# Optimization experiments

Measured on AMD Instinct MI355X. Metric: run time of the kernel, lower is better.

Reference implementation:

```python
import jax, jax.numpy as jnp
import numpy as np

STRIDES = (4, 8, 16, 32, 64, 128)
MAPS = (128, 64, 32, 16, 8, 4)
VAR0, VAR1 = 0.1, 0.2
CLS_TH, NMS_TH, FINAL_TH = 0.05, 0.3, 0.5


def _decode_scale(ocls, oreg, stride):
    # ocls: [1,2,H,W], oreg: [1,4,H,W] -> dets [H*W, 5] = (x1,y1,x2,y2,score)
    prob = jax.nn.softmax(ocls, axis=1)[0, 1]          # [H,W] face probability
    H, W = prob.shape
    s = jnp.float32(stride)
    pcx = s / 2 + jnp.arange(W, dtype=jnp.float32)[None, :] * s   # prior center x
    pcy = s / 2 + jnp.arange(H, dtype=jnp.float32)[:, None] * s   # prior center y
    pwh = s * 4.0                                                 # prior w = h = 4*stride
    loc = oreg[0]                                                 # [4,H,W]
    cx = pcx + loc[0] * VAR0 * pwh
    cy = pcy + loc[1] * VAR0 * pwh
    w = pwh * jnp.exp(loc[2] * VAR1)
    h = pwh * jnp.exp(loc[3] * VAR1)
    x1 = cx - w / 2
    y1 = cy - h / 2
    x2 = x1 + w
    y2 = y1 + h
    return jnp.stack([x1.ravel(), y1.ravel(), x2.ravel(), y2.ravel(), prob.ravel()], axis=1)


def _nms_keep(dets, valid):
    # Greedy NMS (torch-style, +1 box convention), fixed trip count, returns keep mask.
    N = dets.shape[0]
    scores = jnp.where(valid, dets[:, 4], -jnp.inf)
    order = jnp.argsort(-scores)            # descending by score, invalid last
    b = dets[order]
    v = valid[order]
    x1, y1, x2, y2 = b[:, 0], b[:, 1], b[:, 2], b[:, 3]
    areas = (x2 - x1 + 1.0) * (y2 - y1 + 1.0)
    pos = jnp.arange(N)

    def body(i, carry):
        sup, keep = carry
        active = jnp.logical_and(jnp.logical_not(sup[i]), v[i])
        keep = keep.at[i].set(active)
        xx1 = jnp.maximum(x1[i], x1)
        yy1 = jnp.maximum(y1[i], y1)
        xx2 = jnp.minimum(x2[i], x2)
        yy2 = jnp.minimum(y2[i], y2)
        w = jnp.maximum(xx2 - xx1 + 1.0, 0.0)
        h = jnp.maximum(yy2 - yy1 + 1.0, 0.0)
        inter = w * h
        iou = inter / (areas[i] + areas - inter)
        sup = sup | (active & (iou > NMS_TH) & (pos > i))
        return sup, keep

    sup0 = jnp.logical_not(v)
    _, keep_sorted = jax.lax.fori_loop(0, N, body, (sup0, jnp.zeros(N, dtype=bool)))
    return jnp.zeros(N, dtype=bool).at[order].set(keep_sorted)


def _forward(ol1, ol2, ol3, ol4, ol5, ol6, ol7, ol8, ol9, ol10, ol11, ol12):
    olist = [ol1, ol2, ol3, ol4, ol5, ol6, ol7, ol8, ol9, ol10, ol11, ol12]
    dets = jnp.concatenate(
        [_decode_scale(olist[2 * i], olist[2 * i + 1], STRIDES[i]) for i in range(6)],
        axis=0)                              # [N,5]
    valid = dets[:, 4] > CLS_TH              # threshold stage (score > 0.05)
    # NMS selection is index logic -> constant w.r.t. differentiation
    keep = _nms_keep(jax.lax.stop_gradient(dets), valid)
    final = keep & (dets[:, 4] > FINAL_TH)   # post-NMS score > 0.5 filter
    # fixed-shape equivalent of gathering kept rows: zero out non-kept rows
    return dets * final[:, None].astype(dets.dtype)


def setup_inputs() -> dict:
    key = jax.random.key(0)
    inp = {}
    for i, hw in enumerate(MAPS):
        kc, kr, key = jax.random.split(key, 3)
        inp[f"ol{2 * i + 1}"] = jax.random.normal(kc, (1, 2, hw, hw), dtype=jnp.float32)
        inp[f"ol{2 * i + 2}"] = jax.random.normal(kr, (1, 4, hw, hw), dtype=jnp.float32)
    return inp


def reference(ol1, ol2, ol3, ol4, ol5, ol6, ol7, ol8, ol9, ol10, ol11, ol12):
    return _forward(ol1, ol2, ol3, ol4, ol5, ol6, ol7, ol8, ol9, ol10, ol11, ol12)
```

## Files before the change

kernel.cpp:

```cpp
#include <hip/hip_runtime.h>
#include <stdint.h>

#define N_TOTAL 21840
#define NA      21888
#define W_MAX   342
#define TOT_ENT 3753792u
#define NMS_TH  0.3f
#define FINAL_TH 0.5f
#define NSLICE  8
#define SLOTS   11
#define SCAN_T  768
#define GRP     4
#define NBAND   7

struct Inputs { const float* cls[6]; const float* reg[6]; };

__device__ __forceinline__ void block_bar() {
  asm volatile("s_waitcnt lgkmcnt(0)\n\ts_barrier" ::: "memory");
}

__device__ __forceinline__ unsigned rowbase_u(unsigned r) {
  unsigned w = r >> 6, l = r & 63u;
  return 64u * (342u * w - (w * (w - 1u)) / 2u) + l * (342u - w);
}

__global__ void decode_kernel(Inputs in,
                              float* __restrict__ dx1, float* __restrict__ dy1,
                              float* __restrict__ dx2, float* __restrict__ dy2,
                              float* __restrict__ dsc,
                              unsigned long long* __restrict__ ckey,
                              unsigned int* __restrict__ Mc,
                              unsigned int* __restrict__ rank32,
                              unsigned int* __restrict__ cnt,
                              float* __restrict__ out) {
#pragma clang fp contract(off)
  int gid = blockIdx.x * blockDim.x + threadIdx.x;
  if (gid >= N_TOTAL) return;

  rank32[gid] = 0u;
  cnt[gid] = 0u;
  if (gid < NA - N_TOTAL) cnt[N_TOTAL + gid] = 0u;

  int sc, local;
  if      (gid < 16384) { sc = 0; local = gid;         }
  else if (gid < 20480) { sc = 1; local = gid - 16384; }
  else if (gid < 21504) { sc = 2; local = gid - 20480; }
  else if (gid < 21760) { sc = 3; local = gid - 21504; }
  else if (gid < 21824) { sc = 4; local = gid - 21760; }
  else                  { sc = 5; local = gid - 21824; }

  const int Wd     = 128 >> sc;
  const int stride = 4 << sc;
  const int HW     = Wd * Wd;
  const int x = local & (Wd - 1);
  const int y = local >> (7 - sc);

  const float* cls = in.cls[sc];
  const float* reg = in.reg[sc];

  float c0 = cls[local];
  float c1 = cls[HW + local];
  float m  = fmaxf(c0, c1);
  float e0 = expf(c0 - m);
  float e1 = expf(c1 - m);
  float prob = e1 / (e0 + e1);

  float l0 = reg[local];
  float l1 = reg[HW + local];
  float l2 = reg[2 * HW + local];
  float l3 = reg[3 * HW + local];

  float sF  = (float)stride;
  float pcx = 0.5f * sF + (float)x * sF;
  float pcy = 0.5f * sF + (float)y * sF;
  float pwh = sF * 4.0f;

  float cx = pcx + ((l0 * 0.1f) * pwh);
  float cy = pcy + ((l1 * 0.1f) * pwh);
  float w  = pwh * expf(l2 * 0.2f);
  float h  = pwh * expf(l3 * 0.2f);
  float x1 = cx - w * 0.5f;
  float y1 = cy - h * 0.5f;
  float x2 = x1 + w;
  float y2 = y1 + h;

  dx1[gid] = x1; dy1[gid] = y1; dx2[gid] = x2; dy2[gid] = y2; dsc[gid] = prob;

  out[gid * 5 + 0] = 0.0f;
  out[gid * 5 + 1] = 0.0f;
  out[gid * 5 + 2] = 0.0f;
  out[gid * 5 + 3] = 0.0f;
  out[gid * 5 + 4] = 0.0f;

  if (prob > FINAL_TH) {
    unsigned int pos = atomicAdd(Mc, 1u);
    ckey[pos] = ((unsigned long long)__float_as_uint(prob) << 32) |
                (unsigned int)(~(unsigned int)gid);
  }
}

__global__ void __launch_bounds__(256)
rank_kernel(const unsigned long long* __restrict__ ckey,
            const unsigned int* __restrict__ Mc,
            const float* __restrict__ dx1, const float* __restrict__ dy1,
            const float* __restrict__ dx2, const float* __restrict__ dy2,
            float* __restrict__ sx1, float* __restrict__ sy1,
            float* __restrict__ sx2, float* __restrict__ sy2,
            unsigned int* __restrict__ sorig,
            unsigned int* __restrict__ rank32) {
  __shared__ unsigned long long tile[256];
  const unsigned int M = *Mc;
  if (blockIdx.x * 256u >= M) return;
  const int t = (int)threadIdx.x;
  const int p = (int)blockIdx.x * 256 + t;
  unsigned long long mykey = (p < (int)M) ? ckey[p] : 0ull;
  const int S  = (int)((M + NSLICE - 1) / NSLICE);
  const int lo = (int)blockIdx.y * S;
  const int hi = min((int)M, lo + S);
  int partial = 0;
  const int nt = (hi > lo) ? ((hi - lo + 255) >> 8) : 0;
  for (int ti = 0; ti < nt; ++ti) {
    int j = lo + ti * 256 + t;
    tile[t] = (j < hi) ? ckey[j] : 0ull;
    __syncthreads();
#pragma unroll 8
    for (int q = 0; q < 256; ++q) partial += (tile[q] > mykey) ? 1 : 0;
    __syncthreads();
  }
  if (p < (int)M) {
    unsigned int pack = (unsigned int)partial | (1u << 24);
    unsigned int old  = atomicAdd(&rank32[p], pack);
    unsigned int newv = old + pack;
    if ((newv >> 24) == NSLICE) {
      int r = (int)(newv & 0xFFFFFF);
      unsigned int orig = ~(unsigned int)(mykey & 0xffffffffull);
      sx1[r] = dx1[orig];
      sy1[r] = dy1[orig];
      sx2[r] = dx2[orig];
      sy2[r] = dy2[orig];
      sorig[r] = orig;
    }
  }
}

__global__ void __launch_bounds__(1024)
pairs_kernel(const float* __restrict__ sx1, const float* __restrict__ sy1,
             const float* __restrict__ sx2, const float* __restrict__ sy2,
             const unsigned int* __restrict__ Mc,
             unsigned long long* __restrict__ diag,
             unsigned long long* __restrict__ bandT,
             unsigned int* __restrict__ cnt,
             unsigned short* __restrict__ rlJw,
             unsigned long long* __restrict__ rlBits) {
#pragma clang fp contract(off)
  const int M = (int)*Mc;
  const int W = (M + 63) >> 6;
  const int rw = (int)blockIdx.y;
  const int cwg = (int)blockIdx.x << 4;
  if (rw >= W || cwg >= W || cwg + 22 < rw) return;

  const int t = (int)threadIdx.x;
  const int g = t >> 6, l = t & 63;
  const int cw = cwg + g;

  __shared__ float cx1[1024], cy1[1024], cx2[1024], cy2[1024], car[1024];
  {
    int c = (cw << 6) + l;
    if (cw < W && c < M) {
      float a = sx1[c], b = sy1[c], d = sx2[c], e = sy2[c];
      cx1[t] = a; cy1[t] = b; cx2[t] = d; cy2[t] = e;
      car[t] = (d - a + 1.0f) * (e - b + 1.0f);
    }
  }
  __syncthreads();
  if (cw >= W) return;
  const int rwg = rw >> 2, cg = cw >> 2;
  const bool isDiag = (cw == rw);
  const bool isBand = (cw < rw) && (cg >= rwg - 1);
  const bool isCsr  = (cg >= rwg + 2);
  if (!isDiag && !isBand && !isCsr) return;

  const int r = (rw << 6) + l;
  unsigned long long bits = 0ull;
  if (r < M) {
    float ax1 = sx1[r], ay1 = sy1[r], ax2 = sx2[r], ay2 = sy2[r];
    float aarea = (ax2 - ax1 + 1.0f) * (ay2 - ay1 + 1.0f);
    const int cmax = min(64, M - (cw << 6));
    const int sb = g << 6;
    for (int cc = 0; cc < cmax; ++cc) {
      float xx1 = fmaxf(ax1, cx1[sb + cc]);
      float yy1 = fmaxf(ay1, cy1[sb + cc]);
      float xx2 = fminf(ax2, cx2[sb + cc]);
      float yy2 = fminf(ay2, cy2[sb + cc]);
      float ww = fmaxf(xx2 - xx1 + 1.0f, 0.0f);
      float hh = fmaxf(yy2 - yy1 + 1.0f, 0.0f);
      float inter = ww * hh;
      float iou = inter / (aarea + car[sb + cc] - inter);
      if (iou > NMS_TH) bits |= (1ull << cc);
    }
  }
  if (isDiag)      diag[r] = bits;
  else if (isBand) bandT[(size_t)(rw - cw - 1) * NA + r] = bits;
  else if (bits != 0ull) {
    unsigned k = atomicAdd(&cnt[r], 1u);
    unsigned b = rowbase_u((unsigned)r) + k;
    rlJw[b]   = (unsigned short)cw;
    rlBits[b] = bits;
  }
}

__global__ void __launch_bounds__(SCAN_T)
scan_kernel(const unsigned long long* __restrict__ diag,
            const unsigned long long* __restrict__ bandT,
            const unsigned int* __restrict__ cnt,
            const unsigned short* __restrict__ rlJw,
            const unsigned long long* __restrict__ rlBits,
            const unsigned int* __restrict__ sorig,
            const unsigned int* __restrict__ Mc,
            const float* __restrict__ dx1, const float* __restrict__ dy1,
            const float* __restrict__ dx2, const float* __restrict__ dy2,
            const float* __restrict__ dsc,
            float* __restrict__ out) {
  __shared__ unsigned long long sup[W_MAX];
  __shared__ unsigned long long kmls[W_MAX];
  const int t = (int)threadIdx.x;
  const int g = t >> 6, l = t & 63;
  const int M = (int)*Mc;
  const int W = (M + 63) >> 6;
  const int NS = (W + 3) >> 2;

  for (int i = t; i < W_MAX; i += SCAN_T) { sup[i] = 0ull; kmls[i] = 0ull; }
  block_bar();

  if (g == 0) {
    const unsigned long long lowm = (1ull << l) - 1ull;
    unsigned long long dc[4], dn[4];
    unsigned long long bc[4][NBAND], bn[4][NBAND];
    unsigned long long kp[4] = {0ull, 0ull, 0ull, 0ull}, kc[4];
#pragma unroll
    for (int i = 0; i < 4; ++i) {
      int v = i, vc = (v < W) ? v : 0;
      dc[i] = diag[(vc << 6) + l];
#pragma unroll
      for (int d = 1; d <= NBAND; ++d)
        if (d <= i + 4) bc[i][d - 1] = bandT[(size_t)(d - 1) * NA + (vc << 6) + l];
    }
#pragma unroll
    for (int i = 0; i < 4; ++i) {
      int v = 4 + i, vc = (v < W) ? v : 0;
      dn[i] = diag[(vc << 6) + l];
#pragma unroll
      for (int d = 1; d <= NBAND; ++d)
        if (d <= i + 4) bn[i][d - 1] = bandT[(size_t)(d - 1) * NA + (vc << 6) + l];
    }
    for (int s = 0; s < NS; ++s) {
      const int v0 = s << 2;
      unsigned long long sv[4];
#pragma unroll
      for (int i = 0; i < 4; ++i)
        sv[i] = (v0 + i < W) ? sup[v0 + i] : 0ull;
#pragma unroll
      for (int i = 0; i < 4; ++i) {
        const int v = v0 + i;
        unsigned long long kept = 0ull;
        if (v < W) {
          unsigned long long acc = 0ull;
#pragma unroll
          for (int d = 1; d <= NBAND; ++d)
            if (d <= i + 4) {
              unsigned long long src = (d <= i) ? kc[i - d] : kp[i - d + 4];
              acc |= (bc[i][d - 1] & src);
            }
          unsigned long long incoming = __ballot(acc != 0ull);
          const int n = min(64, M - (v << 6));
          unsigned long long wm = (n >= 64) ? ~0ull : ((1ull << n) - 1ull);
          unsigned long long pend = (~(sv[i] | incoming)) & wm;
          const unsigned long long dv = dc[i] & lowm;
          unsigned long long dead = ~pend, und = pend;
          while (und) {
            unsigned long long bS = __ballot((dv & kept) != 0ull) & und;
            unsigned long long bK = __ballot((dv & ~dead) == 0ull) & und;
            kept |= bK; dead |= bS; und &= ~(bK | bS);
          }
          if (l == i) kmls[v] = kept;
        }
        kc[i] = kept;
      }
#pragma unroll
      for (int i = 0; i < 4; ++i) kp[i] = kc[i];
#pragma unroll
      for (int i = 0; i < 4; ++i) {
        dc[i] = dn[i];
#pragma unroll
        for (int d = 0; d < NBAND; ++d)
          if (d <= i + 3) bc[i][d] = bn[i][d];
      }
      const int vn = v0 + 8;
#pragma unroll
      for (int i = 0; i < 4; ++i) {
        int v = vn + i, vc = (v < W) ? v : 0;
        dn[i] = diag[(vc << 6) + l];
#pragma unroll
        for (int d = 1; d <= NBAND; ++d)
          if (d <= i + 4) bn[i][d - 1] = bandT[(size_t)(d - 1) * NA + (vc << 6) + l];
      }
      block_bar();
    }
  } else {
    const int p = (g - 1) * 64 + l;
    const int jrow = p / SLOTS;
    const int sub  = p % SLOTS;
    unsigned cc[4], nc[4];
    unsigned long long cb[4], nb[4];
    unsigned cj[4], nj[4];
#pragma unroll
    for (int i = 0; i < 4; ++i) {
      int w = i, wc = (w < W) ? w : 0;
      cc[i] = cnt[(wc << 6) + jrow];
      unsigned idx = rowbase_u((unsigned)((wc << 6) + jrow)) + sub;
      if (idx >= TOT_ENT) idx = 0;
      cb[i] = rlBits[idx]; cj[i] = (unsigned)rlJw[idx];
    }
#pragma unroll
    for (int i = 0; i < 4; ++i) {
      int w = 4 + i, wc = (w < W) ? w : 0;
      nc[i] = cnt[(wc << 6) + jrow];
      unsigned idx = rowbase_u((unsigned)((wc << 6) + jrow)) + sub;
      if (idx >= TOT_ENT) idx = 0;
      nb[i] = rlBits[idx]; nj[i] = (unsigned)rlJw[idx];
    }
    for (int s = 0; s < NS; ++s) {
      block_bar();
      const int v0 = s << 2;
#pragma unroll
      for (int i = 0; i < 4; ++i) {
        const int w = v0 + i;
        const unsigned long long km = (w < W) ? kmls[w] : 0ull;
        if ((km >> jrow) & 1ull) {
          if (sub < (int)cc[i]) atomicOr(&sup[cj[i]], cb[i]);
          if (cc[i] > (unsigned)SLOTS) {
            unsigned rb_ = rowbase_u((unsigned)((w << 6) + jrow));
            for (int k = sub + SLOTS; k < (int)cc[i]; k += SLOTS) {
              unsigned ii2 = rb_ + k;
              atomicOr(&sup[rlJw[ii2]], rlBits[ii2]);
            }
          }
        }
      }
#pragma unroll
      for (int i = 0; i < 4; ++i) { cc[i] = nc[i]; cb[i] = nb[i]; cj[i] = nj[i]; }
      const int w0 = v0 + 8;
#pragma unroll
      for (int i = 0; i < 4; ++i) {
        int w = w0 + i, wc = (w < W) ? w : 0;
        nc[i] = cnt[(wc << 6) + jrow];
        unsigned idx = rowbase_u((unsigned)((wc << 6) + jrow)) + sub;
        if (idx >= TOT_ENT) idx = 0;
        nb[i] = rlBits[idx]; nj[i] = (unsigned)rlJw[idx];
      }
    }
  }
  block_bar();

  for (int i = t; i < (W << 6); i += SCAN_T) {
    if ((kmls[i >> 6] >> (i & 63)) & 1ull) {
      unsigned int orig = sorig[i];
      out[(size_t)orig * 5 + 0] = dx1[orig];
      out[(size_t)orig * 5 + 1] = dy1[orig];
      out[(size_t)orig * 5 + 2] = dx2[orig];
      out[(size_t)orig * 5 + 3] = dy2[orig];
      out[(size_t)orig * 5 + 4] = dsc[orig];
    }
  }
}

__global__ void __launch_bounds__(1024)
nms_kernel(const float* __restrict__ sx1, const float* __restrict__ sy1,
           const float* __restrict__ sx2, const float* __restrict__ sy2,
           const unsigned int* __restrict__ sorig,
           const unsigned int* __restrict__ Mc,
           unsigned int* __restrict__ keepflag) {
#pragma clang fp contract(off)
  __shared__ unsigned long long sup[W_MAX];
  __shared__ unsigned long long inrow[64];
  __shared__ float wx1[64], wy1[64], wx2[64], wy2[64], warea[64];
  __shared__ unsigned long long keptmask_sh;

  const int t = (int)threadIdx.x;
  const int M = (int)*Mc;
  const int W = (M + 63) >> 6;

  for (int i = t; i < W_MAX; i += 1024) sup[i] = 0ull;
  __syncthreads();

  for (int w = 0; w < W; ++w) {
    const int base = w << 6;
    const int n = min(64, M - base);
    if (t < 64) {
      if (t < n) {
        float a = sx1[base + t], b = sy1[base + t];
        float c = sx2[base + t], d = sy2[base + t];
        wx1[t] = a; wy1[t] = b; wx2[t] = c; wy2[t] = d;
        warea[t] = (c - a + 1.0f) * (d - b + 1.0f);
      }
    } else if (t < 128) {
      inrow[t - 64] = 0ull;
    }
    __syncthreads();
    {
      int r = t & 63, seg = t >> 6;
      unsigned long long bits = 0ull;
      if (r < n) {
        float ax1 = wx1[r], ay1 = wy1[r], ax2 = wx2[r], ay2 = wy2[r];
        float aarea = warea[r];
        for (int c = seg * 4; c < seg * 4 + 4; ++c) {
          if (c > r && c < n) {
            float xx1 = fmaxf(ax1, wx1[c]);
            float yy1 = fmaxf(ay1, wy1[c]);
            float xx2 = fminf(ax2, wx2[c]);
            float yy2 = fminf(ay2, wy2[c]);
            float ww = fmaxf(xx2 - xx1 + 1.0f, 0.0f);
            float hh = fmaxf(yy2 - yy1 + 1.0f, 0.0f);
            float inter = ww * hh;
            float iou = inter / (aarea + warea[c] - inter);
            if (iou > NMS_TH) bits |= (1ull << c);
          }
        }
      }
      if (bits) atomicOr(&inrow[r], bits);
    }
    __syncthreads();
    if (t < 64) {
      unsigned long long wordmask = (n >= 64) ? ~0ull : ((1ull << n) - 1ull);
      unsigned long long pending = (~sup[w]) & wordmask;
      unsigned long long kept = 0ull;
      while (pending) {
        int i = __builtin_ctzll(pending);
        kept |= (1ull << i);
        pending &= ~(inrow[i] | (1ull << i));
      }
      if (t == 0) keptmask_sh = kept;
      if (t < n && ((kept >> t) & 1ull)) keepflag[sorig[base + t]] = 1u;
    }
    __syncthreads();
    unsigned long long km = keptmask_sh;
    if (km) {
      int wid = t >> 6, lane = t & 63;
      for (int jw = w + 1 + wid; (jw << 6) < M; jw += 16) {
        int j = (jw << 6) + lane;
        bool supj = false;
        if (j < M) {
          float jx1 = sx1[j], jy1 = sy1[j], jx2 = sx2[j], jy2 = sy2[j];
          float jarea = (jx2 - jx1 + 1.0f) * (jy2 - jy1 + 1.0f);
          unsigned long long mm = km;
          while (mm) {
            int r = __builtin_ctzll(mm);
            mm &= mm - 1ull;
            float xx1 = fmaxf(wx1[r], jx1);
            float yy1 = fmaxf(wy1[r], jy1);
            float xx2 = fminf(wx2[r], jx2);
            float yy2 = fminf(wy2[r], jy2);
            float ww = fmaxf(xx2 - xx1 + 1.0f, 0.0f);
            float hh = fmaxf(yy2 - yy1 + 1.0f, 0.0f);
            float inter = ww * hh;
            float iou = inter / (warea[r] + jarea - inter);
            if (iou > NMS_TH) { supj = true; break; }
          }
        }
        unsigned long long bal = __ballot(supj);
        if (lane == 0 && bal) atomicOr(&sup[jw], bal);
      }
    }
    __syncthreads();
  }
}

__global__ void output_kernel(const float* __restrict__ dx1, const float* __restrict__ dy1,
                              const float* __restrict__ dx2, const float* __restrict__ dy2,
                              const float* __restrict__ dsc,
                              const unsigned int* __restrict__ keepflag,
                              float* __restrict__ out) {
#pragma clang fp contract(off)
  int gid = blockIdx.x * blockDim.x + threadIdx.x;
  if (gid >= N_TOTAL) return;
  float f = keepflag[gid] ? 1.0f : 0.0f;
  out[gid * 5 + 0] = dx1[gid] * f;
  out[gid * 5 + 1] = dy1[gid] * f;
  out[gid * 5 + 2] = dx2[gid] * f;
  out[gid * 5 + 3] = dy2[gid] * f;
  out[gid * 5 + 4] = dsc[gid] * f;
}

extern "C" void kernel_launch(void* const* d_in, const int* in_sizes, int n_in,
                              void* d_out, int out_size, void* d_ws, size_t ws_size,
                              hipStream_t stream) {
  (void)in_sizes; (void)n_in; (void)out_size;

  Inputs in;
  for (int i = 0; i < 6; ++i) {
    in.cls[i] = (const float*)d_in[2 * i];
    in.reg[i] = (const float*)d_in[2 * i + 1];
  }

  char* ws = (char*)d_ws;
  size_t o = 0;
  float* dx1 = (float*)(ws + o); o += (size_t)NA * 4;
  float* dy1 = (float*)(ws + o); o += (size_t)NA * 4;
  float* dx2 = (float*)(ws + o); o += (size_t)NA * 4;
  float* dy2 = (float*)(ws + o); o += (size_t)NA * 4;
  float* dsc = (float*)(ws + o); o += (size_t)NA * 4;
  unsigned long long* ckey = (unsigned long long*)(ws + o); o += (size_t)NA * 8;
  float* sx1 = (float*)(ws + o); o += (size_t)NA * 4;
  float* sy1 = (float*)(ws + o); o += (size_t)NA * 4;
  float* sx2 = (float*)(ws + o); o += (size_t)NA * 4;
  float* sy2 = (float*)(ws + o); o += (size_t)NA * 4;
  unsigned int* sorig = (unsigned int*)(ws + o); o += (size_t)NA * 4;
  unsigned int* keepflag = (unsigned int*)(ws + o); o += (size_t)NA * 4;
  unsigned int* rank32 = (unsigned int*)(ws + o); o += (size_t)NA * 4;
  unsigned int* cnt = (unsigned int*)(ws + o); o += (size_t)NA * 4;
  unsigned int* Mc = (unsigned int*)(ws + o); o += 64;
  o = (o + 511) & ~(size_t)511;
  unsigned long long* diag = (unsigned long long*)(ws + o); o += (size_t)NA * 8;
  unsigned long long* bandT = (unsigned long long*)(ws + o); o += (size_t)NBAND * NA * 8;
  unsigned long long* rlBits = (unsigned long long*)(ws + o); o += (size_t)TOT_ENT * 8;
  unsigned short* rlJw = (unsigned short*)(ws + o); o += (size_t)TOT_ENT * 2;
  size_t need = o;
  const bool fast = (need <= ws_size);

  const int nb = (N_TOTAL + 255) / 256;

  if (fast) {
    (void)hipMemsetAsync((void*)Mc, 0, 64, stream);
    decode_kernel<<<nb, 256, 0, stream>>>(in, dx1, dy1, dx2, dy2, dsc, ckey, Mc,
                                          rank32, cnt, (float*)d_out);
    rank_kernel<<<dim3(nb, NSLICE), 256, 0, stream>>>(ckey, Mc, dx1, dy1, dx2, dy2,
                                                      sx1, sy1, sx2, sy2, sorig,
                                                      rank32);
    pairs_kernel<<<dim3(22, W_MAX), 1024, 0, stream>>>(sx1, sy1, sx2, sy2, Mc,
                                                       diag, bandT, cnt, rlJw, rlBits);
    scan_kernel<<<1, SCAN_T, 0, stream>>>(diag, bandT, cnt, rlJw, rlBits, sorig, Mc,
                                          dx1, dy1, dx2, dy2, dsc, (float*)d_out);
  } else {
    (void)hipMemsetAsync((void*)keepflag, 0, (size_t)NA * 12 + 64, stream);
    decode_kernel<<<nb, 256, 0, stream>>>(in, dx1, dy1, dx2, dy2, dsc, ckey, Mc,
                                          rank32, cnt, (float*)d_out);
    rank_kernel<<<dim3(nb, NSLICE), 256, 0, stream>>>(ckey, Mc, dx1, dy1, dx2, dy2,
                                                      sx1, sy1, sx2, sy2, sorig,
                                                      rank32);
    nms_kernel<<<1, 1024, 0, stream>>>(sx1, sy1, sx2, sy2, sorig, Mc, keepflag);
    output_kernel<<<nb, 256, 0, stream>>>(dx1, dy1, dx2, dy2, dsc, keepflag,
                                          (float*)d_out);
  }
}
```

Measured before the change: 262.1 us.

## Replace per-step block barriers with LDS flag handshakes between scan producer and pushers

The scan kernel's leader wavefront and the pusher wavefronts no longer meet at a block barrier on every step. They now signal through shared-memory counters: the leader publishes a step flag, and each pusher increments a per-step done counter. The leader only waits for the pushes from two steps back, and it precomputes the band contributions that come from the previous group before it waits. The leader also raises its wave priority, and pushers sleep while polling. This is meant to take barrier stalls off the serial critical path, at the cost of relying on LDS ordering and on the spin loops being correct.

```diff
diff --git a/kernel.cpp b/kernel.cpp
--- a/kernel.cpp
+++ b/kernel.cpp
@@ -10,8 +10,10 @@
 #define NSLICE  8
 #define SLOTS   11
 #define SCAN_T  768
+#define NPUSH   11
 #define GRP     4
 #define NBAND   7
+#define GMAX    86
 
 struct Inputs { const float* cls[6]; const float* reg[6]; };
 
@@ -223,6 +225,8 @@
             float* __restrict__ out) {
   __shared__ unsigned long long sup[W_MAX];
   __shared__ unsigned long long kmls[W_MAX];
+  __shared__ unsigned gdone[GMAX];
+  __shared__ volatile unsigned sflag;
   const int t = (int)threadIdx.x;
   const int g = t >> 6, l = t & 63;
   const int M = (int)*Mc;
@@ -230,13 +234,16 @@
   const int NS = (W + 3) >> 2;
 
   for (int i = t; i < W_MAX; i += SCAN_T) { sup[i] = 0ull; kmls[i] = 0ull; }
+  for (int i = t; i < GMAX; i += SCAN_T) gdone[i] = 0u;
+  if (t == 0) sflag = 0u;
   block_bar();
 
   if (g == 0) {
+    __builtin_amdgcn_s_setprio(1);
     const unsigned long long lowm = (1ull << l) - 1ull;
     unsigned long long dc[4], dn[4];
     unsigned long long bc[4][NBAND], bn[4][NBAND];
-    unsigned long long kp[4] = {0ull, 0ull, 0ull, 0ull}, kc[4];
+    unsigned long long kp[4] = {0ull, 0ull, 0ull, 0ull};
 #pragma unroll
     for (int i = 0; i < 4; ++i) {
       int v = i, vc = (v < W) ? v : 0;
@@ -255,22 +262,33 @@
     }
     for (int s = 0; s < NS; ++s) {
       const int v0 = s << 2;
+      unsigned long long accp[4];
+#pragma unroll
+      for (int i = 0; i < 4; ++i) {
+        unsigned long long a = 0ull;
+#pragma unroll
+        for (int d = 1; d <= NBAND; ++d)
+          if (d <= i + 4 && d > i) a |= (bc[i][d - 1] & kp[i - d + 4]);
+        accp[i] = a;
+      }
+      if (s >= 2) {
+        while (*(volatile unsigned*)&gdone[s - 2] < (unsigned)NPUSH) {}
+        asm volatile("" ::: "memory");
+      }
       unsigned long long sv[4];
 #pragma unroll
       for (int i = 0; i < 4; ++i)
         sv[i] = (v0 + i < W) ? sup[v0 + i] : 0ull;
+      unsigned long long kc[4];
 #pragma unroll
       for (int i = 0; i < 4; ++i) {
         const int v = v0 + i;
         unsigned long long kept = 0ull;
         if (v < W) {
-          unsigned long long acc = 0ull;
-#pragma unroll
-          for (int d = 1; d <= NBAND; ++d)
-            if (d <= i + 4) {
-              unsigned long long src = (d <= i) ? kc[i - d] : kp[i - d + 4];
-              acc |= (bc[i][d - 1] & src);
-            }
+          unsigned long long acc = accp[i];
+#pragma unroll
+          for (int d = 1; d <= 3; ++d)
+            if (d <= i) acc |= (bc[i][d - 1] & kc[i - d]);
           unsigned long long incoming = __ballot(acc != 0ull);
           const int n = min(64, M - (v << 6));
           unsigned long long wm = (n >= 64) ? ~0ull : ((1ull << n) - 1ull);
@@ -286,6 +304,8 @@
         }
         kc[i] = kept;
       }
+      asm volatile("s_waitcnt lgkmcnt(0)" ::: "memory");
+      if (l == 0) sflag = (unsigned)(s + 1);
 #pragma unroll
       for (int i = 0; i < 4; ++i) kp[i] = kc[i];
 #pragma unroll
@@ -304,8 +324,8 @@
         for (int d = 1; d <= NBAND; ++d)
           if (d <= i + 4) bn[i][d - 1] = bandT[(size_t)(d - 1) * NA + (vc << 6) + l];
       }
-      block_bar();
-    }
+    }
+    __builtin_amdgcn_s_setprio(0);
   } else {
     const int p = (g - 1) * 64 + l;
     const int jrow = p / SLOTS;
@@ -330,7 +350,8 @@
       nb[i] = rlBits[idx]; nj[i] = (unsigned)rlJw[idx];
     }
     for (int s = 0; s < NS; ++s) {
-      block_bar();
+      while (sflag < (unsigned)(s + 1)) __builtin_amdgcn_s_sleep(1);
+      asm volatile("" ::: "memory");
       const int v0 = s << 2;
 #pragma unroll
       for (int i = 0; i < 4; ++i) {
@@ -347,6 +368,8 @@
           }
         }
       }
+      asm volatile("s_waitcnt lgkmcnt(0)" ::: "memory");
+      if (l == 0) atomicAdd(&gdone[s], 1u);
 #pragma unroll
       for (int i = 0; i < 4; ++i) { cc[i] = nc[i]; cb[i] = nb[i]; cj[i] = nj[i]; }
       const int w0 = v0 + 8;
```

After: 260.8 us. About the same (-0.5%).
